# Performance work log

Hardware: AMD Instinct MI355X
Metric: run time of the kernel (lower is better)

## Reference

```python
import jax, jax.numpy as jnp
import numpy as np

N_NODES = 50000
N_EDGES = 800000


def setup_inputs() -> dict:
    key = jax.random.key(0)
    ks = jax.random.split(key, 8)
    feats = jax.random.normal(ks[0], (N_NODES, 256), dtype=jnp.float32)
    src = jax.random.randint(ks[1], (N_EDGES,), 0, N_NODES, dtype=jnp.int32)
    dst = jax.random.randint(ks[2], (N_EDGES,), 0, N_NODES, dtype=jnp.int32)
    # Glorot-ish init for GraphConv weights
    W0 = jax.random.normal(ks[3], (256, 256), dtype=jnp.float32) * (1.0 / 16.0)
    W1 = jax.random.normal(ks[4], (256, 256), dtype=jnp.float32) * (1.0 / 16.0)
    W2 = jax.random.normal(ks[5], (256, 128), dtype=jnp.float32) * (1.0 / 16.0)
    b0 = jnp.zeros((256,), dtype=jnp.float32)
    b1 = jnp.zeros((256,), dtype=jnp.float32)
    b2 = jnp.zeros((128,), dtype=jnp.float32)
    return {"feats": feats, "src": src, "dst": dst,
            "W0": W0, "b0": b0, "W1": W1, "b1": b1, "W2": W2, "b2": b2}


def _graph_conv(x, src, dst, W, b, activate):
    """DGL GraphConv with norm='both': h = D_in^{-1/2} A D_out^{-1/2} x W + b."""
    n = x.shape[0]
    e_ones = jnp.ones(src.shape[0], dtype=x.dtype)
    deg_out = jax.ops.segment_sum(e_ones, src, num_segments=n)  # out-degree (src norm)
    deg_in = jax.ops.segment_sum(e_ones, dst, num_segments=n)   # in-degree (dst norm)
    norm_src = jnp.where(deg_out > 0, deg_out, 1.0) ** -0.5
    norm_dst = jnp.where(deg_in > 0, deg_in, 1.0) ** -0.5
    h = x * norm_src[:, None]
    # transform first (in_feats >= out_feats path in DGL) then aggregate
    h = h @ W
    m = jax.ops.segment_sum(h[src], dst, num_segments=n)  # [N, out] neighbor sum
    h = m * norm_dst[:, None] + b
    if activate:
        h = jax.nn.relu(h)
    return h


def reference(feats, src, dst, W0, b0, W1, b1, W2, b2):
    # dropout is identity in eval mode
    h0 = _graph_conv(feats, src, dst, W0, b0, True)
    h1 = _graph_conv(h0, src, dst, W1, b1, True)
    h2 = _graph_conv(h1, src, dst, W2, b2, False)  # last layer: no activation
    return (h0, h1, h2, h2)  # (h_list..., h)
```

## Files before the change

kernel.cpp:

```cpp
#include <hip/hip_runtime.h>
#include <hip/hip_bf16.h>

#define NN 50000
#define NE 800000
#define MPAD 50048
#define NBLK 196
#define BSTR 64

typedef __attribute__((ext_vector_type(8))) short short8;
typedef __attribute__((ext_vector_type(4))) float f32x4;
typedef __attribute__((ext_vector_type(4))) unsigned short us4;
typedef __attribute__((ext_vector_type(8))) unsigned short us8;

static __device__ __forceinline__ unsigned short f2bf(float f) {
    union { float f; unsigned int u; } v; v.f = f;
    unsigned int u = v.u;
    return (unsigned short)((u + 0x7FFFu + ((u >> 16) & 1u)) >> 16);
}
static __device__ __forceinline__ float bf2f(unsigned short h) {
    union { unsigned int u; float f; } v; v.u = ((unsigned int)h) << 16;
    return v.f;
}

__global__ void k_degsort(const int* __restrict__ src, const int* __restrict__ dst,
                          int* __restrict__ degO, int* __restrict__ degI,
                          int* __restrict__ bucket) {
    int e = blockIdx.x * 256 + threadIdx.x;
    if (e < NE) {
        int s = src[e], d = dst[e];
        atomicAdd(&degO[s], 1);
        int p = atomicAdd(&degI[d], 1);
        bucket[d * BSTR + p] = s;
    }
}

__global__ void k_norm(const int* __restrict__ degO, const int* __restrict__ degI,
                       float* __restrict__ nS, float* __restrict__ nD) {
    int i = blockIdx.x * 256 + threadIdx.x;
    if (i < NN) {
        int o = degO[i], d = degI[i];
        nS[i] = 1.0f / sqrtf((float)(o > 0 ? o : 1));
        nD[i] = 1.0f / sqrtf((float)(d > 0 ? d : 1));
    }
}

__global__ void k_cvtW3T(const float* __restrict__ W0, const float* __restrict__ W1,
                         const float* __restrict__ W2,
                         unsigned short* __restrict__ W0T, unsigned short* __restrict__ W1T,
                         unsigned short* __restrict__ W2T) {
    int i = blockIdx.x * 256 + threadIdx.x;
    if (i < 65536) {
        int k = i >> 8, c = i & 255;
        W0T[c * 256 + k] = f2bf(W0[i]);
    } else if (i < 131072) {
        int j = i - 65536;
        int k = j >> 8, c = j & 255;
        W1T[c * 256 + k] = f2bf(W1[j]);
    } else if (i < 163840) {
        int j = i - 131072;
        int k = j >> 7, c = j & 127;
        W2T[c * 256 + k] = f2bf(W2[j]);
    }
}

__global__ void k_cvt0(const float* __restrict__ x, const float* __restrict__ nS,
                       unsigned short* __restrict__ xb) {
    int row = blockIdx.x; int t = threadIdx.x;
    float s = nS[row];
    xb[(long)row * 256 + t] = f2bf(x[(long)row * 256 + t] * s);
}

__global__ __launch_bounds__(256) void k_aggb(const int* __restrict__ degI,
                                              const int* __restrict__ bucket,
                                              const unsigned short* __restrict__ xb,
                                              const float* __restrict__ nD,
                                              unsigned short* __restrict__ aggb) {
    const int node = blockIdx.x * 4 + (threadIdx.x >> 6);
    const int lane = threadIdx.x & 63;
    const int half = lane >> 5;
    const int c = (lane & 31) * 8;
    if (node >= NN) {
        if (node < MPAD && half == 0)
            *(us8*)&aggb[(long)node * 256 + c] = (us8){0,0,0,0,0,0,0,0};
        return;
    }
    const int e0 = node * BSTR;
    const int e1 = e0 + degI[node];
    float acc[8] = {0.f,0.f,0.f,0.f,0.f,0.f,0.f,0.f};
    int j = e0;
    for (; j + 4 <= e1; j += 4) {
        int sA = __builtin_nontemporal_load(&bucket[j + half]);
        int sB = __builtin_nontemporal_load(&bucket[j + 2 + half]);
        us8 vA = *(const us8*)&xb[(long)sA * 256 + c];
        us8 vB = *(const us8*)&xb[(long)sB * 256 + c];
#pragma unroll
        for (int k = 0; k < 8; k++) acc[k] += bf2f(vA[k]) + bf2f(vB[k]);
    }
    if (j + 2 <= e1) {
        int sA = __builtin_nontemporal_load(&bucket[j + half]);
        us8 vA = *(const us8*)&xb[(long)sA * 256 + c];
#pragma unroll
        for (int k = 0; k < 8; k++) acc[k] += bf2f(vA[k]);
        j += 2;
    }
    if (j < e1 && half == 0) {
        int sA = __builtin_nontemporal_load(&bucket[j]);
        us8 vA = *(const us8*)&xb[(long)sA * 256 + c];
#pragma unroll
        for (int k = 0; k < 8; k++) acc[k] += bf2f(vA[k]);
    }
#pragma unroll
    for (int k = 0; k < 8; k++) acc[k] += __shfl_xor(acc[k], 32, 64);
    if (half == 0) {
        float nd = nD[node];
        us8 o;
#pragma unroll
        for (int k = 0; k < 8; k++) o[k] = f2bf(acc[k] * nd);
        *(us8*)&aggb[(long)node * 256 + c] = o;
    }
}

template<int NOUT, int MODE>
__global__ __launch_bounds__(256) void k_gemm(const unsigned short* __restrict__ A,
                                              const unsigned short* __restrict__ BT,
                                              const float* __restrict__ bias,
                                              const float* __restrict__ nS,
                                              float* __restrict__ outF,
                                              unsigned short* __restrict__ xbn,
                                              unsigned short* __restrict__ outB) {
    __shared__ unsigned short As[128][40];
    __shared__ unsigned short Bs[128][36];
    const int bm = blockIdx.x * 128;
    const int bn = blockIdx.y * 128;
    const int tid = threadIdx.x;
    const int lane = tid & 63;
    const int w = tid >> 6;
    const int wr = w >> 1, wc = w & 1;

    f32x4 acc[4][4];
#pragma unroll
    for (int m = 0; m < 4; m++)
#pragma unroll
        for (int n = 0; n < 4; n++) acc[m][n] = (f32x4){0.f, 0.f, 0.f, 0.f};

    for (int kt = 0; kt < 256; kt += 32) {
        {
            int r = tid >> 1, c = (tid & 1) * 16;
            const unsigned short* g = &A[(long)(bm + r) * 256 + kt + c];
            *(us8*)&As[r][c]     = *(const us8*)(g);
            *(us8*)&As[r][c + 8] = *(const us8*)(g + 8);
        }
        {
            int col = tid >> 1, kh = (tid & 1) * 16;
            const unsigned short* g = &BT[(long)(bn + col) * 256 + kt + kh];
            *(us8*)&Bs[col][kh]     = *(const us8*)(g);
            *(us8*)&Bs[col][kh + 8] = *(const us8*)(g + 8);
        }
        __syncthreads();

        union U { us4 h[2]; short8 s; };
        const int kb = (lane >> 4) * 4;
        short8 af[4], bf[4];
#pragma unroll
        for (int m = 0; m < 4; m++) {
            int r = wr * 64 + m * 16 + (lane & 15);
            U u; u.h[0] = *(const us4*)&As[r][kb]; u.h[1] = *(const us4*)&As[r][kb + 16];
            af[m] = u.s;
        }
#pragma unroll
        for (int n = 0; n < 4; n++) {
            int cl = wc * 64 + n * 16 + (lane & 15);
            U u; u.h[0] = *(const us4*)&Bs[cl][kb]; u.h[1] = *(const us4*)&Bs[cl][kb + 16];
            bf[n] = u.s;
        }
#pragma unroll
        for (int m = 0; m < 4; m++)
#pragma unroll
            for (int n = 0; n < 4; n++)
                acc[m][n] = __builtin_amdgcn_mfma_f32_16x16x32_bf16(af[m], bf[n], acc[m][n], 0, 0, 0);
        __syncthreads();
    }

#pragma unroll
    for (int m = 0; m < 4; m++) {
        int rbase = bm + wr * 64 + m * 16 + (lane >> 4) * 4;
#pragma unroll
        for (int n = 0; n < 4; n++) {
            int gc = bn + wc * 64 + n * 16 + (lane & 15);
            float bb = (MODE == 0) ? bias[gc] : 0.f;
#pragma unroll
            for (int j = 0; j < 4; j++) {
                int row = rbase + j;
                if (MODE == 0) {
                    if (row < NN) {
                        float v = fmaxf(acc[m][n][j] + bb, 0.f);
                        __builtin_nontemporal_store(v, &outF[(long)row * 256 + gc]);
                        xbn[(long)row * 256 + gc] = f2bf(v * nS[row]);
                    } else {
                        xbn[(long)row * 256 + gc] = 0;
                    }
                } else {
                    outB[(long)row * NOUT + gc] = f2bf(acc[m][n][j]);
                }
            }
        }
    }
}

__global__ __launch_bounds__(256) void k_agg2(const int* __restrict__ degI,
                                              const int* __restrict__ bucket,
                                              const unsigned short* __restrict__ hgb,
                                              const float* __restrict__ nD,
                                              const float* __restrict__ b,
                                              float* __restrict__ h2,
                                              float* __restrict__ h2b) {
    const int node = blockIdx.x * 4 + (threadIdx.x >> 6);
    const int lane = threadIdx.x & 63;
    if (node >= NN) return;
    const int q = lane >> 4;
    const int c = (lane & 15) * 8;
    const int e0 = node * BSTR;
    const int e1 = e0 + degI[node];
    float acc[8] = {0.f,0.f,0.f,0.f,0.f,0.f,0.f,0.f};
    int j = e0;
    for (; j + 8 <= e1; j += 8) {
        int sA = __builtin_nontemporal_load(&bucket[j + q]);
        int sB = __builtin_nontemporal_load(&bucket[j + 4 + q]);
        us8 vA = *(const us8*)&hgb[(long)sA * 128 + c];
        us8 vB = *(const us8*)&hgb[(long)sB * 128 + c];
#pragma unroll
        for (int k = 0; k < 8; k++) acc[k] += bf2f(vA[k]) + bf2f(vB[k]);
    }
    if (j + 4 <= e1) {
        int sA = __builtin_nontemporal_load(&bucket[j + q]);
        us8 vA = *(const us8*)&hgb[(long)sA * 128 + c];
#pragma unroll
        for (int k = 0; k < 8; k++) acc[k] += bf2f(vA[k]);
        j += 4;
    }
    if (j < e1 && q < (e1 - j)) {
        int sA = __builtin_nontemporal_load(&bucket[j + q]);
        us8 vA = *(const us8*)&hgb[(long)sA * 128 + c];
#pragma unroll
        for (int k = 0; k < 8; k++) acc[k] += bf2f(vA[k]);
    }
#pragma unroll
    for (int k = 0; k < 8; k++) acc[k] += __shfl_xor(acc[k], 16, 64);
#pragma unroll
    for (int k = 0; k < 8; k++) acc[k] += __shfl_xor(acc[k], 32, 64);
    if (q == 0) {
        float nd = nD[node];
        f32x4 v0, v1;
#pragma unroll
        for (int k = 0; k < 4; k++) v0[k] = acc[k] * nd + b[c + k];
#pragma unroll
        for (int k = 0; k < 4; k++) v1[k] = acc[4 + k] * nd + b[c + 4 + k];
        __builtin_nontemporal_store(v0, (f32x4*)&h2[(long)node * 128 + c]);
        __builtin_nontemporal_store(v1, (f32x4*)&h2[(long)node * 128 + c + 4]);
        __builtin_nontemporal_store(v0, (f32x4*)&h2b[(long)node * 128 + c]);
        __builtin_nontemporal_store(v1, (f32x4*)&h2b[(long)node * 128 + c + 4]);
    }
}

extern "C" void kernel_launch(void* const* d_in, const int* in_sizes, int n_in,
                              void* d_out, int out_size, void* d_ws, size_t ws_size,
                              hipStream_t stream) {
    const float* feats = (const float*)d_in[0];
    const int*   src   = (const int*)d_in[1];
    const int*   dst   = (const int*)d_in[2];
    const float* W0 = (const float*)d_in[3];
    const float* b0 = (const float*)d_in[4];
    const float* W1 = (const float*)d_in[5];
    const float* b1 = (const float*)d_in[6];
    const float* W2 = (const float*)d_in[7];
    const float* b2 = (const float*)d_in[8];

    float* out = (float*)d_out;
    float* h0  = out;
    float* h1  = out + (long)NN * 256;
    float* h2  = out + 2L * NN * 256;
    float* h2b = out + 2L * NN * 256 + (long)NN * 128;

    char* ws = (char*)d_ws;
    size_t off = 0;
    auto alloc = [&](size_t bytes) { void* p = ws + off; off += (bytes + 255) & ~255UL; return p; };
    unsigned short* xb   = (unsigned short*)alloc((size_t)MPAD * 256 * 2);
    unsigned short* xb2  = (unsigned short*)alloc((size_t)MPAD * 256 * 2);
    unsigned short* aggb = (unsigned short*)alloc((size_t)MPAD * 256 * 2);
    unsigned short* hgb  = (unsigned short*)alloc((size_t)MPAD * 128 * 2);
    unsigned short* W0T = (unsigned short*)alloc(256 * 256 * 2);
    unsigned short* W1T = (unsigned short*)alloc(256 * 256 * 2);
    unsigned short* W2T = (unsigned short*)alloc(128 * 256 * 2);
    int*   zint   = (int*)alloc((size_t)2 * NN * 4);
    int*   degO   = zint;
    int*   degI   = zint + NN;
    float* nS     = (float*)alloc(NN * 4);
    float* nD     = (float*)alloc(NN * 4);
    int*   bucket = (int*)alloc((size_t)NN * BSTR * 4);

    hipMemsetAsync(zint, 0, (size_t)2 * NN * 4, stream);
    k_degsort<<<(NE + 255) / 256, 256, 0, stream>>>(src, dst, degO, degI, bucket);
    k_norm<<<NBLK, 256, 0, stream>>>(degO, degI, nS, nD);

    k_cvtW3T<<<(163840 + 255) / 256, 256, 0, stream>>>(W0, W1, W2, W0T, W1T, W2T);

    k_cvt0<<<NN, 256, 0, stream>>>(feats, nS, xb);

    k_aggb<<<MPAD / 4, 256, 0, stream>>>(degI, bucket, xb, nD, aggb);
    k_gemm<256, 0><<<dim3(MPAD / 128, 2), 256, 0, stream>>>(aggb, W0T, b0, nS, h0, xb2, nullptr);

    k_aggb<<<MPAD / 4, 256, 0, stream>>>(degI, bucket, xb2, nD, aggb);
    k_gemm<256, 0><<<dim3(MPAD / 128, 2), 256, 0, stream>>>(aggb, W1T, b1, nS, h1, xb, nullptr);

    k_gemm<128, 1><<<dim3(MPAD / 128, 1), 256, 0, stream>>>(xb, W2T, nullptr, nullptr, nullptr, nullptr, hgb);
    k_agg2<<<(NN + 3) / 4, 256, 0, stream>>>(degI, bucket, hgb, nD, b2, h2, h2b);
}
```

Before: 361.9 us.

## Fuse prep kernels and load neighbor lists once per wave with shuffles

Merges the norm, weight-transpose and feature-conversion kernels into one launch that computes the degree norms inline. The aggregation kernels now load the node's whole bucket row with one coalesced read per lane and hand indices out with wave shuffles, instead of issuing per-edge index loads. k_aggb also changes to four edge groups of 16 channels each. The aims are fewer launches, fewer dependent index loads and more gathers in flight per wave. In exchange it uses more registers for 16 accumulators, adds extra shuffle reductions, and reads the full 64-entry bucket row even for low-degree nodes.

```diff
diff --git a/kernel.cpp b/kernel.cpp
--- a/kernel.cpp
+++ b/kernel.cpp
@@ -4,7 +4,6 @@
 #define NN 50000
 #define NE 800000
 #define MPAD 50048
-#define NBLK 196
 #define BSTR 64
 
 typedef __attribute__((ext_vector_type(8))) short short8;
@@ -34,40 +33,37 @@
     }
 }
 
-__global__ void k_norm(const int* __restrict__ degO, const int* __restrict__ degI,
-                       float* __restrict__ nS, float* __restrict__ nD) {
-    int i = blockIdx.x * 256 + threadIdx.x;
-    if (i < NN) {
-        int o = degO[i], d = degI[i];
-        nS[i] = 1.0f / sqrtf((float)(o > 0 ? o : 1));
-        nD[i] = 1.0f / sqrtf((float)(d > 0 ? d : 1));
-    }
-}
-
-__global__ void k_cvtW3T(const float* __restrict__ W0, const float* __restrict__ W1,
-                         const float* __restrict__ W2,
-                         unsigned short* __restrict__ W0T, unsigned short* __restrict__ W1T,
-                         unsigned short* __restrict__ W2T) {
-    int i = blockIdx.x * 256 + threadIdx.x;
-    if (i < 65536) {
-        int k = i >> 8, c = i & 255;
-        W0T[c * 256 + k] = f2bf(W0[i]);
-    } else if (i < 131072) {
-        int j = i - 65536;
-        int k = j >> 8, c = j & 255;
-        W1T[c * 256 + k] = f2bf(W1[j]);
-    } else if (i < 163840) {
-        int j = i - 131072;
-        int k = j >> 7, c = j & 127;
-        W2T[c * 256 + k] = f2bf(W2[j]);
-    }
-}
-
-__global__ void k_cvt0(const float* __restrict__ x, const float* __restrict__ nS,
-                       unsigned short* __restrict__ xb) {
-    int row = blockIdx.x; int t = threadIdx.x;
-    float s = nS[row];
-    xb[(long)row * 256 + t] = f2bf(x[(long)row * 256 + t] * s);
+__global__ void k_prep(const float* __restrict__ x,
+                       const int* __restrict__ degO, const int* __restrict__ degI,
+                       float* __restrict__ nS, float* __restrict__ nD,
+                       unsigned short* __restrict__ xb,
+                       const float* __restrict__ W0, const float* __restrict__ W1,
+                       const float* __restrict__ W2,
+                       unsigned short* __restrict__ W0T, unsigned short* __restrict__ W1T,
+                       unsigned short* __restrict__ W2T) {
+    int bid = blockIdx.x;
+    int t = threadIdx.x;
+    if (bid < NN) {
+        int o = degO[bid], d = degI[bid];
+        float ns = 1.0f / sqrtf((float)(o > 0 ? o : 1));
+        float nd = 1.0f / sqrtf((float)(d > 0 ? d : 1));
+        if (t == 0) { nS[bid] = ns; nD[bid] = nd; }
+        xb[(long)bid * 256 + t] = f2bf(x[(long)bid * 256 + t] * ns);
+    } else {
+        int i = (bid - NN) * 256 + t;
+        if (i < 65536) {
+            int k = i >> 8, c = i & 255;
+            W0T[c * 256 + k] = f2bf(W0[i]);
+        } else if (i < 131072) {
+            int j = i - 65536;
+            int k = j >> 8, c = j & 255;
+            W1T[c * 256 + k] = f2bf(W1[j]);
+        } else {
+            int j = i - 131072;
+            int k = j >> 7, c = j & 127;
+            W2T[c * 256 + k] = f2bf(W2[j]);
+        }
+    }
 }
 
 __global__ __launch_bounds__(256) void k_aggb(const int* __restrict__ degI,
@@ -77,46 +73,70 @@
                                               unsigned short* __restrict__ aggb) {
     const int node = blockIdx.x * 4 + (threadIdx.x >> 6);
     const int lane = threadIdx.x & 63;
-    const int half = lane >> 5;
-    const int c = (lane & 31) * 8;
+    const int q = lane >> 4;
+    const int cl = (lane & 15) * 16;
     if (node >= NN) {
-        if (node < MPAD && half == 0)
-            *(us8*)&aggb[(long)node * 256 + c] = (us8){0,0,0,0,0,0,0,0};
+        if (node < MPAD && q == 0) {
+            us8 z = {0,0,0,0,0,0,0,0};
+            *(us8*)&aggb[(long)node * 256 + cl] = z;
+            *(us8*)&aggb[(long)node * 256 + cl + 8] = z;
+        }
         return;
     }
-    const int e0 = node * BSTR;
-    const int e1 = e0 + degI[node];
-    float acc[8] = {0.f,0.f,0.f,0.f,0.f,0.f,0.f,0.f};
-    int j = e0;
-    for (; j + 4 <= e1; j += 4) {
-        int sA = __builtin_nontemporal_load(&bucket[j + half]);
-        int sB = __builtin_nontemporal_load(&bucket[j + 2 + half]);
-        us8 vA = *(const us8*)&xb[(long)sA * 256 + c];
-        us8 vB = *(const us8*)&xb[(long)sB * 256 + c];
-#pragma unroll
-        for (int k = 0; k < 8; k++) acc[k] += bf2f(vA[k]) + bf2f(vB[k]);
-    }
-    if (j + 2 <= e1) {
-        int sA = __builtin_nontemporal_load(&bucket[j + half]);
-        us8 vA = *(const us8*)&xb[(long)sA * 256 + c];
-#pragma unroll
-        for (int k = 0; k < 8; k++) acc[k] += bf2f(vA[k]);
-        j += 2;
-    }
-    if (j < e1 && half == 0) {
-        int sA = __builtin_nontemporal_load(&bucket[j]);
-        us8 vA = *(const us8*)&xb[(long)sA * 256 + c];
-#pragma unroll
-        for (int k = 0; k < 8; k++) acc[k] += bf2f(vA[k]);
-    }
-#pragma unroll
-    for (int k = 0; k < 8; k++) acc[k] += __shfl_xor(acc[k], 32, 64);
-    if (half == 0) {
+    const int deg = degI[node];
+    const int bidx = bucket[node * BSTR + lane];
+    float acc[16];
+#pragma unroll
+    for (int k = 0; k < 16; k++) acc[k] = 0.f;
+    int j = 0;
+    for (; j + 8 <= deg; j += 8) {
+        int s0 = __shfl(bidx, j + q, 64);
+        int s1 = __shfl(bidx, j + 4 + q, 64);
+        const unsigned short* g0 = &xb[(long)s0 * 256 + cl];
+        const unsigned short* g1 = &xb[(long)s1 * 256 + cl];
+        us8 a0 = *(const us8*)g0;
+        us8 a1 = *(const us8*)(g0 + 8);
+        us8 b0 = *(const us8*)g1;
+        us8 b1 = *(const us8*)(g1 + 8);
+#pragma unroll
+        for (int k = 0; k < 8; k++) {
+            acc[k]     += bf2f(a0[k]) + bf2f(b0[k]);
+            acc[8 + k] += bf2f(a1[k]) + bf2f(b1[k]);
+        }
+    }
+    if (j + 4 <= deg) {
+        int s0 = __shfl(bidx, j + q, 64);
+        const unsigned short* g0 = &xb[(long)s0 * 256 + cl];
+        us8 a0 = *(const us8*)g0;
+        us8 a1 = *(const us8*)(g0 + 8);
+#pragma unroll
+        for (int k = 0; k < 8; k++) { acc[k] += bf2f(a0[k]); acc[8 + k] += bf2f(a1[k]); }
+        j += 4;
+    }
+    if (j < deg) {
+        int s0 = __shfl(bidx, j + q, 64);
+        if (q < deg - j) {
+            const unsigned short* g0 = &xb[(long)s0 * 256 + cl];
+            us8 a0 = *(const us8*)g0;
+            us8 a1 = *(const us8*)(g0 + 8);
+#pragma unroll
+            for (int k = 0; k < 8; k++) { acc[k] += bf2f(a0[k]); acc[8 + k] += bf2f(a1[k]); }
+        }
+    }
+#pragma unroll
+    for (int k = 0; k < 16; k++) acc[k] += __shfl_xor(acc[k], 16, 64);
+#pragma unroll
+    for (int k = 0; k < 16; k++) acc[k] += __shfl_xor(acc[k], 32, 64);
+    if (q == 0) {
         float nd = nD[node];
-        us8 o;
-#pragma unroll
-        for (int k = 0; k < 8; k++) o[k] = f2bf(acc[k] * nd);
-        *(us8*)&aggb[(long)node * 256 + c] = o;
+        us8 o0, o1;
+#pragma unroll
+        for (int k = 0; k < 8; k++) {
+            o0[k] = f2bf(acc[k] * nd);
+            o1[k] = f2bf(acc[8 + k] * nd);
+        }
+        *(us8*)&aggb[(long)node * 256 + cl] = o0;
+        *(us8*)&aggb[(long)node * 256 + cl + 8] = o1;
     }
 }
 
@@ -218,31 +238,35 @@
     const int lane = threadIdx.x & 63;
     if (node >= NN) return;
     const int q = lane >> 4;
-    const int c = (lane & 15) * 8;
-    const int e0 = node * BSTR;
-    const int e1 = e0 + degI[node];
-    float acc[8] = {0.f,0.f,0.f,0.f,0.f,0.f,0.f,0.f};
-    int j = e0;
-    for (; j + 8 <= e1; j += 8) {
-        int sA = __builtin_nontemporal_load(&bucket[j + q]);
-        int sB = __builtin_nontemporal_load(&bucket[j + 4 + q]);
-        us8 vA = *(const us8*)&hgb[(long)sA * 128 + c];
-        us8 vB = *(const us8*)&hgb[(long)sB * 128 + c];
+    const int cl = (lane & 15) * 8;
+    const int deg = degI[node];
+    const int bidx = bucket[node * BSTR + lane];
+    float acc[8];
+#pragma unroll
+    for (int k = 0; k < 8; k++) acc[k] = 0.f;
+    int j = 0;
+    for (; j + 8 <= deg; j += 8) {
+        int s0 = __shfl(bidx, j + q, 64);
+        int s1 = __shfl(bidx, j + 4 + q, 64);
+        us8 vA = *(const us8*)&hgb[(long)s0 * 128 + cl];
+        us8 vB = *(const us8*)&hgb[(long)s1 * 128 + cl];
 #pragma unroll
         for (int k = 0; k < 8; k++) acc[k] += bf2f(vA[k]) + bf2f(vB[k]);
     }
-    if (j + 4 <= e1) {
-        int sA = __builtin_nontemporal_load(&bucket[j + q]);
-        us8 vA = *(const us8*)&hgb[(long)sA * 128 + c];
+    if (j + 4 <= deg) {
+        int s0 = __shfl(bidx, j + q, 64);
+        us8 vA = *(const us8*)&hgb[(long)s0 * 128 + cl];
 #pragma unroll
         for (int k = 0; k < 8; k++) acc[k] += bf2f(vA[k]);
         j += 4;
     }
-    if (j < e1 && q < (e1 - j)) {
-        int sA = __builtin_nontemporal_load(&bucket[j + q]);
-        us8 vA = *(const us8*)&hgb[(long)sA * 128 + c];
-#pragma unroll
-        for (int k = 0; k < 8; k++) acc[k] += bf2f(vA[k]);
+    if (j < deg) {
+        int s0 = __shfl(bidx, j + q, 64);
+        if (q < deg - j) {
+            us8 vA = *(const us8*)&hgb[(long)s0 * 128 + cl];
+#pragma unroll
+            for (int k = 0; k < 8; k++) acc[k] += bf2f(vA[k]);
+        }
     }
 #pragma unroll
     for (int k = 0; k < 8; k++) acc[k] += __shfl_xor(acc[k], 16, 64);
@@ -252,13 +276,13 @@
         float nd = nD[node];
         f32x4 v0, v1;
 #pragma unroll
-        for (int k = 0; k < 4; k++) v0[k] = acc[k] * nd + b[c + k];
-#pragma unroll
-        for (int k = 0; k < 4; k++) v1[k] = acc[4 + k] * nd + b[c + 4 + k];
-        __builtin_nontemporal_store(v0, (f32x4*)&h2[(long)node * 128 + c]);
-        __builtin_nontemporal_store(v1, (f32x4*)&h2[(long)node * 128 + c + 4]);
-        __builtin_nontemporal_store(v0, (f32x4*)&h2b[(long)node * 128 + c]);
-        __builtin_nontemporal_store(v1, (f32x4*)&h2b[(long)node * 128 + c + 4]);
+        for (int k = 0; k < 4; k++) v0[k] = acc[k] * nd + b[cl + k];
+#pragma unroll
+        for (int k = 0; k < 4; k++) v1[k] = acc[4 + k] * nd + b[cl + 4 + k];
+        __builtin_nontemporal_store(v0, (f32x4*)&h2[(long)node * 128 + cl]);
+        __builtin_nontemporal_store(v1, (f32x4*)&h2[(long)node * 128 + cl + 4]);
+        __builtin_nontemporal_store(v0, (f32x4*)&h2b[(long)node * 128 + cl]);
+        __builtin_nontemporal_store(v1, (f32x4*)&h2b[(long)node * 128 + cl + 4]);
     }
 }
 
@@ -300,11 +324,9 @@
 
     hipMemsetAsync(zint, 0, (size_t)2 * NN * 4, stream);
     k_degsort<<<(NE + 255) / 256, 256, 0, stream>>>(src, dst, degO, degI, bucket);
-    k_norm<<<NBLK, 256, 0, stream>>>(degO, degI, nS, nD);
-
-    k_cvtW3T<<<(163840 + 255) / 256, 256, 0, stream>>>(W0, W1, W2, W0T, W1T, W2T);
-
-    k_cvt0<<<NN, 256, 0, stream>>>(feats, nS, xb);
+
+    k_prep<<<NN + 640, 256, 0, stream>>>(feats, degO, degI, nS, nD, xb,
+                                         W0, W1, W2, W0T, W1T, W2T);
 
     k_aggb<<<MPAD / 4, 256, 0, stream>>>(degI, bucket, xb, nD, aggb);
     k_gemm<256, 0><<<dim3(MPAD / 128, 2), 256, 0, stream>>>(aggb, W0T, b0, nS, h0, xb2, nullptr);
```

New measurement: 349.3 us. 1.04x faster.
